# Performance work log

Measured on AMD Instinct MI355X. Metric: run time of the kernel, lower is better.

## Reference

```python
import jax, jax.numpy as jnp
import numpy as np

EMBED_DIM = 1024
NUM_HEADS = 16
HEAD_DIM = EMBED_DIM // NUM_HEADS
ROPE_THETA = 10000.0


def setup_inputs() -> dict:
    key = jax.random.key(0)
    k1, k2, k3, k4, k5 = jax.random.split(key, 5)
    B, S, E = 2, 2048, EMBED_DIM
    scale = 1.0 / np.sqrt(E)
    x = jax.random.normal(k1, (B, S, E), dtype=jnp.float32)
    w_qkv = jax.random.normal(k2, (E, 3 * E), dtype=jnp.float32) * scale
    b_qkv = jnp.zeros((3 * E,), dtype=jnp.float32)
    w_o = jax.random.normal(k3, (E, E), dtype=jnp.float32) * scale
    b_o = jnp.zeros((E,), dtype=jnp.float32)
    return {"x": x, "w_qkv": w_qkv, "b_qkv": b_qkv, "w_o": w_o, "b_o": b_o}


def _rope_cos_sin(seq_len, dtype):
    # half-dim frequencies, GPT-NeoX rotate-half convention
    inv_freq = 1.0 / (ROPE_THETA ** (jnp.arange(0, HEAD_DIM, 2, dtype=jnp.float32) / HEAD_DIM))
    pos = jnp.arange(seq_len, dtype=jnp.float32)
    freqs = pos[:, None] * inv_freq[None, :]          # [S, hd/2]
    emb = jnp.concatenate([freqs, freqs], axis=-1)    # [S, hd]
    return jnp.cos(emb).astype(dtype), jnp.sin(emb).astype(dtype)


def _rotate_half(t):
    t1, t2 = jnp.split(t, 2, axis=-1)
    return jnp.concatenate([-t2, t1], axis=-1)


def reference(x, w_qkv, b_qkv, w_o, b_o):
    B, S, E = x.shape
    H, D = NUM_HEADS, HEAD_DIM
    qkv = x @ w_qkv + b_qkv                            # [B, S, 3E]
    q, k, v = jnp.split(qkv, 3, axis=-1)
    # [B, H, S, D]
    q = q.reshape(B, S, H, D).transpose(0, 2, 1, 3)
    k = k.reshape(B, S, H, D).transpose(0, 2, 1, 3)
    v = v.reshape(B, S, H, D).transpose(0, 2, 1, 3)
    cos, sin = _rope_cos_sin(S, x.dtype)               # [S, D]
    q = q * cos + _rotate_half(q) * sin
    k = k * cos + _rotate_half(k) * sin
    scores = jnp.einsum('bhqd,bhkd->bhqk', q, k) / jnp.sqrt(jnp.asarray(D, x.dtype))
    causal = jnp.tril(jnp.ones((S, S), dtype=bool))
    scores = jnp.where(causal, scores, jnp.asarray(-1e30, x.dtype))
    attn = jax.nn.softmax(scores, axis=-1)
    out = jnp.einsum('bhqk,bhkd->bhqd', attn, v)       # [B, H, S, D]
    out = out.transpose(0, 2, 1, 3).reshape(B, S, E)
    return out @ w_o + b_o
```

## Files before the change

### kernel.cpp

```cpp
#include <hip/hip_runtime.h>
#include <hip/hip_bf16.h>

typedef __hip_bfloat16 bf16_t;
typedef __attribute__((ext_vector_type(8))) __bf16 bf16x8;
typedef __attribute__((ext_vector_type(4))) float f32x4;
typedef __attribute__((ext_vector_type(4))) unsigned short ushort4v;
typedef __attribute__((ext_vector_type(4))) short short4v;

#define NUM_B 2
#define NUM_H 16
#define SEQ   2048
#define EMB   1024
#define LOG2E 1.44269504088896340736f
#define LN10K 13.287712379549449f

__global__ __launch_bounds__(256) void prep_kernel(
    const float* __restrict__ x, const float* __restrict__ wq,
    const float* __restrict__ wo, bf16_t* __restrict__ xb,
    bf16_t* __restrict__ wqT, bf16_t* __restrict__ woT) {
  __shared__ float tile[32][33];
  int bid = blockIdx.x, tid = threadIdx.x;
  if (bid < 4096) {
    int i = (bid * 256 + tid) * 4;
    f32x4 v = *(const f32x4*)&x[i];
    ushort4v p;
#pragma unroll
    for (int j = 0; j < 4; ++j)
      p[j] = __builtin_bit_cast(unsigned short, __float2bfloat16(v[j]));
    *(ushort4v*)&xb[i] = p;
    return;
  }
  const float* src;
  bf16_t* dst;
  int R, C, c0, r0;
  if (bid < 4096 + 3072) {
    int b = bid - 4096;
    src = wq; dst = wqT; R = 1024; C = 3072;
    c0 = (b % 96) * 32; r0 = (b / 96) * 32;
  } else {
    int b = bid - 7168;
    src = wo; dst = woT; R = 1024; C = 1024;
    c0 = (b % 32) * 32; r0 = (b / 32) * 32;
  }
  int tx = tid & 31, ty = tid >> 5;
#pragma unroll
  for (int i = 0; i < 4; ++i)
    tile[ty + i * 8][tx] = src[(size_t)(r0 + ty + i * 8) * C + c0 + tx];
  __syncthreads();
#pragma unroll
  for (int i = 0; i < 4; ++i)
    dst[(size_t)(c0 + ty + i * 8) * R + r0 + tx] = __float2bfloat16(tile[tx][ty + i * 8]);
}

__device__ __forceinline__ void stage_half(const bf16_t* __restrict__ G,
                                           int row0, int k0, int ld,
                                           bf16_t* Ls, int tid) {
#pragma unroll
  for (int r = 0; r < 2; ++r) {
    int c = tid + r * 512;
    int row = c >> 3, g = c & 7;
    const char* gp = (const char*)(G + (size_t)(row0 + row) * ld + k0) +
                     ((g ^ (row & 7)) * 16);
    char* lp = (char*)Ls + c * 16;
    __builtin_amdgcn_global_load_lds((const __attribute__((address_space(1))) void*)gp,
                                     (__attribute__((address_space(3))) void*)lp, 16, 0, 0);
  }
}

__global__ __launch_bounds__(512, 2) void gemm_qkv_8ph(
    const bf16_t* __restrict__ A, const bf16_t* __restrict__ Bt,
    const float* __restrict__ bias, bf16_t* __restrict__ out0,
    bf16_t* __restrict__ out1, bf16_t* __restrict__ out2) {
  __shared__ __align__(16) bf16_t As[2][256 * 64];
  __shared__ __align__(16) bf16_t Bs[2][256 * 64];
  const int Kd = 1024;
  const int NT = 16;
  int tid = threadIdx.x;
  int wave = tid >> 6, lane = tid & 63;
  int lr = lane & 15, lq = lane >> 4;
  int wm = wave >> 2, wn = wave & 3;
  int m0 = blockIdx.x * 256, n0 = blockIdx.y * 256;
  int sw = lr & 7;
  int gk0 = (lq ^ sw) * 16;
  int gk1 = ((4 + lq) ^ sw) * 16;

  f32x4 acc[8][4];
#pragma unroll
  for (int i = 0; i < 8; ++i)
#pragma unroll
    for (int j = 0; j < 4; ++j) acc[i][j] = (f32x4){0.f, 0.f, 0.f, 0.f};

  stage_half(A, m0, 0, Kd, &As[0][0], tid);
  stage_half(A, m0 + 128, 0, Kd, &As[0][128 * 64], tid);
  stage_half(Bt, n0, 0, Kd, &Bs[0][0], tid);
  stage_half(Bt, n0 + 128, 0, Kd, &Bs[0][128 * 64], tid);
  stage_half(A, m0, 64, Kd, &As[1][0], tid);
  asm volatile("s_waitcnt vmcnt(2)" ::: "memory");
  __builtin_amdgcn_s_barrier();

  bf16x8 af[4][2], blo[2][2], bhi[2][2];
  int aw = wm * 128, bw = wn * 64;

#pragma unroll 2
  for (int t = 0; t < NT; ++t) {
    int cur = t & 1, nxt = cur ^ 1;
    const char* Ac = (const char*)As[cur];
    const char* Bc = (const char*)Bs[cur];

#pragma unroll
    for (int mi = 0; mi < 4; ++mi) {
      int ro = (aw + mi * 16 + lr) * 128;
      af[mi][0] = *(const bf16x8*)(Ac + ro + gk0);
      af[mi][1] = *(const bf16x8*)(Ac + ro + gk1);
    }
#pragma unroll
    for (int nj = 0; nj < 2; ++nj) {
      int ro = (bw + nj * 16 + lr) * 128;
      blo[nj][0] = *(const bf16x8*)(Bc + ro + gk0);
      blo[nj][1] = *(const bf16x8*)(Bc + ro + gk1);
    }
    if (t + 1 < NT) stage_half(A, m0 + 128, (t + 1) * 64, Kd, &As[nxt][128 * 64], tid);
    __builtin_amdgcn_s_barrier();
    asm volatile("s_waitcnt lgkmcnt(0)" ::: "memory");
    __builtin_amdgcn_s_setprio(1);
#pragma unroll
    for (int mi = 0; mi < 4; ++mi)
#pragma unroll
      for (int nj = 0; nj < 2; ++nj) {
        acc[mi][nj] = __builtin_amdgcn_mfma_f32_16x16x32_bf16(af[mi][0], blo[nj][0], acc[mi][nj], 0, 0, 0);
        acc[mi][nj] = __builtin_amdgcn_mfma_f32_16x16x32_bf16(af[mi][1], blo[nj][1], acc[mi][nj], 0, 0, 0);
      }
    __builtin_amdgcn_s_setprio(0);
    __builtin_amdgcn_s_barrier();

#pragma unroll
    for (int nj = 0; nj < 2; ++nj) {
      int ro = (bw + (nj + 2) * 16 + lr) * 128;
      bhi[nj][0] = *(const bf16x8*)(Bc + ro + gk0);
      bhi[nj][1] = *(const bf16x8*)(Bc + ro + gk1);
    }
    if (t + 1 < NT) stage_half(Bt, n0, (t + 1) * 64, Kd, &Bs[nxt][0], tid);
    __builtin_amdgcn_s_barrier();
    asm volatile("s_waitcnt lgkmcnt(0)" ::: "memory");
    __builtin_amdgcn_s_setprio(1);
#pragma unroll
    for (int mi = 0; mi < 4; ++mi)
#pragma unroll
      for (int nj = 0; nj < 2; ++nj) {
        acc[mi][nj + 2] = __builtin_amdgcn_mfma_f32_16x16x32_bf16(af[mi][0], bhi[nj][0], acc[mi][nj + 2], 0, 0, 0);
        acc[mi][nj + 2] = __builtin_amdgcn_mfma_f32_16x16x32_bf16(af[mi][1], bhi[nj][1], acc[mi][nj + 2], 0, 0, 0);
      }
    __builtin_amdgcn_s_setprio(0);
    __builtin_amdgcn_s_barrier();

#pragma unroll
    for (int mi = 0; mi < 4; ++mi) {
      int ro = (aw + (mi + 4) * 16 + lr) * 128;
      af[mi][0] = *(const bf16x8*)(Ac + ro + gk0);
      af[mi][1] = *(const bf16x8*)(Ac + ro + gk1);
    }
    if (t + 1 < NT) stage_half(Bt, n0 + 128, (t + 1) * 64, Kd, &Bs[nxt][128 * 64], tid);
    __builtin_amdgcn_s_barrier();
    asm volatile("s_waitcnt lgkmcnt(0)" ::: "memory");
    __builtin_amdgcn_s_setprio(1);
#pragma unroll
    for (int mi = 0; mi < 4; ++mi)
#pragma unroll
      for (int nj = 0; nj < 2; ++nj) {
        acc[mi + 4][nj + 2] = __builtin_amdgcn_mfma_f32_16x16x32_bf16(af[mi][0], bhi[nj][0], acc[mi + 4][nj + 2], 0, 0, 0);
        acc[mi + 4][nj + 2] = __builtin_amdgcn_mfma_f32_16x16x32_bf16(af[mi][1], bhi[nj][1], acc[mi + 4][nj + 2], 0, 0, 0);
      }
    __builtin_amdgcn_s_setprio(0);
    __builtin_amdgcn_s_barrier();

#pragma unroll
    for (int nj = 0; nj < 2; ++nj) {
      int ro = (bw + nj * 16 + lr) * 128;
      blo[nj][0] = *(const bf16x8*)(Bc + ro + gk0);
      blo[nj][1] = *(const bf16x8*)(Bc + ro + gk1);
    }
    if (t + 2 < NT) stage_half(A, m0, (t + 2) * 64, Kd, &As[cur][0], tid);
    __builtin_amdgcn_s_barrier();
    asm volatile("s_waitcnt lgkmcnt(0)" ::: "memory");
    __builtin_amdgcn_s_setprio(1);
#pragma unroll
    for (int mi = 0; mi < 4; ++mi)
#pragma unroll
      for (int nj = 0; nj < 2; ++nj) {
        acc[mi + 4][nj] = __builtin_amdgcn_mfma_f32_16x16x32_bf16(af[mi][0], blo[nj][0], acc[mi + 4][nj], 0, 0, 0);
        acc[mi + 4][nj] = __builtin_amdgcn_mfma_f32_16x16x32_bf16(af[mi][1], blo[nj][1], acc[mi + 4][nj], 0, 0, 0);
      }
    __builtin_amdgcn_s_setprio(0);
    if (t + 1 < NT) {
      if (t + 2 < NT) asm volatile("s_waitcnt vmcnt(2)" ::: "memory");
      else            asm volatile("s_waitcnt vmcnt(0)" ::: "memory");
      __builtin_amdgcn_s_barrier();
    }
  }

#pragma unroll
  for (int pr = 0; pr < 2; ++pr) {
    int na = n0 + wn * 64 + pr * 16 + lr;
    int nb = na + 32;
    int sec = na >> 10;
    int h = (na >> 6) & (NUM_H - 1);
    int da = na & 63;
    float bva = bias[na], bvb = bias[nb];
    if (sec == 2) {
#pragma unroll
      for (int mi = 0; mi < 8; ++mi) {
        int mbase = m0 + wm * 128 + mi * 16 + lq * 4;
        int b = mbase >> 11;
        int s = mbase & (SEQ - 1);
        int bh = b * NUM_H + h;
        ushort4v pa, pb;
#pragma unroll
        for (int r = 0; r < 4; ++r) {
          pa[r] = __builtin_bit_cast(unsigned short, __float2bfloat16(acc[mi][pr][r] + bva));
          pb[r] = __builtin_bit_cast(unsigned short, __float2bfloat16(acc[mi][pr + 2][r] + bvb));
        }
        *(ushort4v*)&out2[((size_t)bh * 64 + da) * SEQ + s] = pa;
        *(ushort4v*)&out2[((size_t)bh * 64 + da + 32) * SEQ + s] = pb;
      }
    } else {
      bf16_t* dst = (sec == 0) ? out0 : out1;
      float scale = (sec == 0) ? 0.125f : 1.0f;
      int i = da & 31;
      float inv = exp2f(-(float)i * (LN10K / 32.0f));
#pragma unroll
      for (int mi = 0; mi < 8; ++mi) {
        int mbase = m0 + wm * 128 + mi * 16 + lq * 4;
        int b = mbase >> 11;
        int s0 = mbase & (SEQ - 1);
        int bh = b * NUM_H + h;
#pragma unroll
        for (int r = 0; r < 4; ++r) {
          float sn, cs;
          sincosf((float)(s0 + r) * inv, &sn, &cs);
          float va = acc[mi][pr][r] + bva;
          float vb = acc[mi][pr + 2][r] + bvb;
          float oa = (va * cs - vb * sn) * scale;
          float ob = (vb * cs + va * sn) * scale;
          size_t rowb = ((size_t)bh * SEQ + (s0 + r)) * 64;
          dst[rowb + da] = __float2bfloat16(oa);
          dst[rowb + da + 32] = __float2bfloat16(ob);
        }
      }
    }
  }
}

template <int CH>
__device__ __forceinline__ void stage_tile(const bf16_t* __restrict__ G,
                                           int row0, int col0, int ld,
                                           bf16_t* Ls, int tid) {
#pragma unroll
  for (int r = 0; r < CH; ++r) {
    int c = tid + r * 256;
    int row = c >> 2, g = c & 3;
    const char* gp = (const char*)(G + (size_t)(row0 + row) * ld + col0) +
                     ((g ^ ((row >> 1) & 3)) * 16);
    char* lp = (char*)Ls + c * 16;
    __builtin_amdgcn_global_load_lds((const __attribute__((address_space(1))) void*)gp,
                                     (__attribute__((address_space(3))) void*)lp, 16, 0, 0);
  }
}

template <int MODE, int MT>
__global__ __launch_bounds__(256) void gemm_bf16_kernel(
    const bf16_t* __restrict__ A, const bf16_t* __restrict__ Bt,
    const float* __restrict__ bias, bf16_t* __restrict__ out0,
    bf16_t* __restrict__ out1, bf16_t* __restrict__ out2,
    float* __restrict__ outf, int Ndim, int Kdim) {
  __shared__ __align__(16) bf16_t As[MT * 32 * 32];
  __shared__ __align__(16) bf16_t Bs[128 * 32];
  int tid = threadIdx.x;
  int wave = tid >> 6, lane = tid & 63;
  int lr = lane & 15, lq = lane >> 4;
  int m0 = blockIdx.x * (32 * MT), n0 = blockIdx.y * 128;
  int wm = (wave >> 1) * (MT * 16), wn = (wave & 1) * 64;
  int key = (lr >> 1) & 3;
  int goff = ((lq ^ key) * 8);
  f32x4 acc[MT][4];
#pragma unroll
  for (int i = 0; i < MT; ++i)
#pragma unroll
    for (int j = 0; j < 4; ++j) acc[i][j] = (f32x4){0.f, 0.f, 0.f, 0.f};

  for (int k0 = 0; k0 < Kdim; k0 += 32) {
    __syncthreads();
    stage_tile<MT / 2>(A, m0, k0, Kdim, As, tid);
    stage_tile<2>(Bt, n0, k0, Kdim, Bs, tid);
    __syncthreads();
    bf16x8 af[MT], bfr[4];
#pragma unroll
    for (int mt = 0; mt < MT; ++mt)
      af[mt] = *(const bf16x8*)&As[(wm + mt * 16 + lr) * 32 + goff];
#pragma unroll
    for (int nt = 0; nt < 4; ++nt)
      bfr[nt] = *(const bf16x8*)&Bs[(wn + nt * 16 + lr) * 32 + goff];
#pragma unroll
    for (int mt = 0; mt < MT; ++mt)
#pragma unroll
      for (int nt = 0; nt < 4; ++nt)
        acc[mt][nt] = __builtin_amdgcn_mfma_f32_16x16x32_bf16(af[mt], bfr[nt], acc[mt][nt], 0, 0, 0);
  }

  if (MODE == 0) {
#pragma unroll
    for (int pr = 0; pr < 2; ++pr) {
      int na = n0 + wn + pr * 16 + lr;
      int nb = na + 32;
      int sec = na >> 10;
      int h = (na >> 6) & (NUM_H - 1);
      int da = na & 63;
      float bva = bias[na], bvb = bias[nb];
      if (sec == 2) {
#pragma unroll
        for (int mt = 0; mt < MT; ++mt) {
          int mbase = m0 + wm + mt * 16 + lq * 4;
          int b = mbase >> 11;
          int s = mbase & (SEQ - 1);
          int bh = b * NUM_H + h;
          ushort4v pa, pb;
#pragma unroll
          for (int r = 0; r < 4; ++r) {
            pa[r] = __builtin_bit_cast(unsigned short, __float2bfloat16(acc[mt][pr][r] + bva));
            pb[r] = __builtin_bit_cast(unsigned short, __float2bfloat16(acc[mt][pr + 2][r] + bvb));
          }
          *(ushort4v*)&out2[((size_t)bh * 64 + da) * SEQ + s] = pa;
          *(ushort4v*)&out2[((size_t)bh * 64 + da + 32) * SEQ + s] = pb;
        }
      } else {
        bf16_t* dst = (sec == 0) ? out0 : out1;
        float scale = (sec == 0) ? 0.125f : 1.0f;
        int i = da & 31;
        float inv = exp2f(-(float)i * (LN10K / 32.0f));
#pragma unroll
        for (int mt = 0; mt < MT; ++mt) {
          int mbase = m0 + wm + mt * 16 + lq * 4;
          int b = mbase >> 11;
          int s0 = mbase & (SEQ - 1);
          int bh = b * NUM_H + h;
#pragma unroll
          for (int r = 0; r < 4; ++r) {
            float sn, cs;
            sincosf((float)(s0 + r) * inv, &sn, &cs);
            float va = acc[mt][pr][r] + bva;
            float vb = acc[mt][pr + 2][r] + bvb;
            float oa = (va * cs - vb * sn) * scale;
            float ob = (vb * cs + va * sn) * scale;
            size_t rowb = ((size_t)bh * SEQ + (s0 + r)) * 64;
            dst[rowb + da] = __float2bfloat16(oa);
            dst[rowb + da + 32] = __float2bfloat16(ob);
          }
        }
      }
    }
  } else {
#pragma unroll
    for (int nt = 0; nt < 4; ++nt) {
      int n = n0 + wn + nt * 16 + lr;
      float bv = bias[n];
#pragma unroll
      for (int mt = 0; mt < MT; ++mt)
#pragma unroll
        for (int r = 0; r < 4; ++r) {
          int m = m0 + wm + mt * 16 + lq * 4 + r;
          outf[(size_t)m * Ndim + n] = acc[mt][nt][r] + bv;
        }
    }
  }
}

__device__ __forceinline__ void stage_sw(const char* __restrict__ gbase,
                                         size_t rowStride, bf16_t* lds, int tid) {
#pragma unroll
  for (int r = 0; r < 2; ++r) {
    int c = tid + r * 256;
    int row = c >> 3, g = c & 7;
    const char* gp = gbase + (size_t)row * rowStride + ((g ^ (row & 7)) * 16);
    char* lp = (char*)lds + c * 16;
    __builtin_amdgcn_global_load_lds((const __attribute__((address_space(1))) void*)gp,
                                     (__attribute__((address_space(3))) void*)lp, 16, 0, 0);
  }
}

__global__ __launch_bounds__(256) void flash_attn_kernel(
    const bf16_t* __restrict__ Q, const bf16_t* __restrict__ K,
    const bf16_t* __restrict__ Vt, bf16_t* __restrict__ O) {
  __shared__ __align__(16) bf16_t Ks[2][64 * 64];
  __shared__ __align__(16) bf16_t Vs[2][64 * 64];
  int tid = threadIdx.x;
  int wv = tid >> 6, lane = tid & 63;
  int lr = lane & 15, lq = lane >> 4;
  int bx = blockIdx.x;
  int bh = bx & 31;
  int tile = 31 - (bx >> 5);
  int qw0 = tile * 64 + wv * 16;
  const bf16_t* Qb = Q + (size_t)bh * SEQ * 64;
  const bf16_t* Kb = K + (size_t)bh * SEQ * 64;
  const bf16_t* Vb = Vt + (size_t)bh * 64 * SEQ;
  int sw = lr & 7;
  int g0 = (lq ^ sw) * 8;
  int g1 = g0 ^ 32;

  bf16x8 aq0 = *(const bf16x8*)&Qb[(size_t)(qw0 + lr) * 64 + lq * 8];
  bf16x8 aq1 = *(const bf16x8*)&Qb[(size_t)(qw0 + lr) * 64 + 32 + lq * 8];

  f32x4 Oacc[4];
#pragma unroll
  for (int dt = 0; dt < 4; ++dt) Oacc[dt] = (f32x4){0.f, 0.f, 0.f, 0.f};
  float lrow = 0.f;

  int nch = tile + 1;
  stage_sw((const char*)Kb, 128, Ks[0], tid);
  stage_sw((const char*)Vb, SEQ * 2, Vs[0], tid);

  for (int ch = 0; ch < nch; ++ch) {
    int cur = ch & 1;
    bool diag = (ch == tile);
    __syncthreads();
    if (ch + 1 < nch) {
      int kvn = (ch + 1) * 64;
      stage_sw((const char*)(Kb + (size_t)kvn * 64), 128, Ks[cur ^ 1], tid);
      stage_sw((const char*)Vb + (size_t)kvn * 2, SEQ * 2, Vs[cur ^ 1], tid);
    }

#pragma unroll
    for (int sub = 0; sub < 4; ++sub) {
      if (!diag || sub <= wv) {
        int rk = (sub * 16 + lr) * 64;
        bf16x8 k0 = *(const bf16x8*)&Ks[cur][rk + g0];
        bf16x8 k1 = *(const bf16x8*)&Ks[cur][rk + g1];
        f32x4 t = (f32x4){0.f, 0.f, 0.f, 0.f};
        t = __builtin_amdgcn_mfma_f32_16x16x32_bf16(k0, aq0, t, 0, 0, 0);
        t = __builtin_amdgcn_mfma_f32_16x16x32_bf16(k1, aq1, t, 0, 0, 0);
        if (diag && sub == wv) {
#pragma unroll
          for (int r = 0; r < 4; ++r)
            if (lq * 4 + r > lr) t[r] = -1e30f;
        }
        short4v pp;
#pragma unroll
        for (int r = 0; r < 4; ++r) {
          float p = exp2f(t[r] * LOG2E);
          lrow += p;
          pp[r] = __builtin_bit_cast(short, __float2bfloat16(p));
        }
#pragma unroll
        for (int dt = 0; dt < 4; ++dt) {
          int row = dt * 16 + lr;
          int grp = (sub * 2 + (lq >> 1)) ^ sw;
          short4v av = *(const short4v*)&Vs[cur][row * 64 + grp * 8 + (lq & 1) * 4];
          Oacc[dt] = __builtin_amdgcn_mfma_f32_16x16x16bf16_1k(av, pp, Oacc[dt], 0, 0, 0);
        }
      }
    }
  }

  lrow += __shfl_xor(lrow, 16, 64);
  lrow += __shfl_xor(lrow, 32, 64);

  int b = bh >> 4, h = bh & (NUM_H - 1);
  int q = qw0 + lr;
  size_t base = (((size_t)b * SEQ + q) * NUM_H + h) * 64;
  float rinv = 1.0f / lrow;
#pragma unroll
  for (int dt = 0; dt < 4; ++dt) {
    ushort4v ok;
#pragma unroll
    for (int r = 0; r < 4; ++r)
      ok[r] = __builtin_bit_cast(unsigned short, __float2bfloat16(Oacc[dt][r] * rinv));
    *(ushort4v*)&O[base + dt * 16 + lq * 4] = ok;
  }
}

extern "C" void kernel_launch(void* const* d_in, const int* in_sizes, int n_in,
                              void* d_out, int out_size, void* d_ws, size_t ws_size,
                              hipStream_t stream) {
  const float* x      = (const float*)d_in[0];
  const float* w_qkv  = (const float*)d_in[1];
  const float* b_qkv  = (const float*)d_in[2];
  const float* w_o    = (const float*)d_in[3];
  const float* b_o    = (const float*)d_in[4];
  float* out = (float*)d_out;

  bf16_t* ws    = (bf16_t*)d_ws;
  bf16_t* xb    = ws;
  bf16_t* wqkvT = xb + 4 * 1024 * 1024;
  bf16_t* woT   = wqkvT + 3072 * 1024;
  bf16_t* Qb    = woT + 1024 * 1024;
  bf16_t* Kb    = Qb + 4 * 1024 * 1024;
  bf16_t* Vt    = Kb + 4 * 1024 * 1024;
  bf16_t* attn  = Vt + 4 * 1024 * 1024;

  prep_kernel<<<8192, 256, 0, stream>>>(x, w_qkv, w_o, xb, wqkvT, woT);
  gemm_qkv_8ph<<<dim3(16, 12), 512, 0, stream>>>(xb, wqkvT, b_qkv, Qb, Kb, Vt);
  flash_attn_kernel<<<1024, 256, 0, stream>>>(Qb, Kb, Vt, attn);
  gemm_bf16_kernel<1, 2><<<dim3(64, 8), 256, 0, stream>>>(
      attn, woT, b_o, nullptr, nullptr, nullptr, out, 1024, 1024);
}
```

Before: 209.7 us.

## Precompute staging addresses and rebalance QKV GEMM prefetch schedule

Replaces the generic half-tile staging helper with per-lane precomputed global and LDS pointers, so each stage is just two global_load_lds calls at fixed offsets. The prefetch schedule is rearranged: the third phase no longer issues loads, and the fourth phase issues both the next A0 and B1 halves two steps ahead. The vmcnt waits are adjusted to match, and the loop unroll is reduced to 1. The QKV epilogue is rewritten to handle both column pairs with shared index math, and the unused MODE==0 epilogue of the generic GEMM is removed. The aim is lower address arithmetic, smaller code size and better load overlap, at the risk of weaker latency hiding because more loads are outstanding at the later barrier.

```diff
diff --git a/kernel.cpp b/kernel.cpp
--- a/kernel.cpp
+++ b/kernel.cpp
@@ -52,19 +52,11 @@
     dst[(size_t)(c0 + ty + i * 8) * R + r0 + tx] = __float2bfloat16(tile[tx][ty + i * 8]);
 }
 
-__device__ __forceinline__ void stage_half(const bf16_t* __restrict__ G,
-                                           int row0, int k0, int ld,
-                                           bf16_t* Ls, int tid) {
-#pragma unroll
-  for (int r = 0; r < 2; ++r) {
-    int c = tid + r * 512;
-    int row = c >> 3, g = c & 7;
-    const char* gp = (const char*)(G + (size_t)(row0 + row) * ld + k0) +
-                     ((g ^ (row & 7)) * 16);
-    char* lp = (char*)Ls + c * 16;
-    __builtin_amdgcn_global_load_lds((const __attribute__((address_space(1))) void*)gp,
-                                     (__attribute__((address_space(3))) void*)lp, 16, 0, 0);
-  }
+__device__ __forceinline__ void stage2(const char* gBase, int kByte, char* ldsLane) {
+  __builtin_amdgcn_global_load_lds((const __attribute__((address_space(1))) void*)(gBase + kByte),
+                                   (__attribute__((address_space(3))) void*)ldsLane, 16, 0, 0);
+  __builtin_amdgcn_global_load_lds((const __attribute__((address_space(1))) void*)(gBase + kByte + 64 * 2048),
+                                   (__attribute__((address_space(3))) void*)(ldsLane + 8192), 16, 0, 0);
 }
 
 __global__ __launch_bounds__(512, 2) void gemm_qkv_8ph(
@@ -73,7 +65,6 @@
     bf16_t* __restrict__ out1, bf16_t* __restrict__ out2) {
   __shared__ __align__(16) bf16_t As[2][256 * 64];
   __shared__ __align__(16) bf16_t Bs[2][256 * 64];
-  const int Kd = 1024;
   const int NT = 16;
   int tid = threadIdx.x;
   int wave = tid >> 6, lane = tid & 63;
@@ -84,28 +75,40 @@
   int gk0 = (lq ^ sw) * 16;
   int gk1 = ((4 + lq) ^ sw) * 16;
 
+  int rowL = tid >> 3, g7 = tid & 7;
+  size_t laneOff = (size_t)rowL * 2048 + ((g7 ^ (rowL & 7)) * 16);
+  const char* A0L = (const char*)(A + (size_t)m0 * 1024) + laneOff;
+  const char* A1L = A0L + 128 * 2048;
+  const char* B0L = (const char*)(Bt + (size_t)n0 * 1024) + laneOff;
+  const char* B1L = B0L + 128 * 2048;
+  char* AsL = (char*)As + (size_t)tid * 16;
+  char* BsL = (char*)Bs + (size_t)tid * 16;
+
   f32x4 acc[8][4];
 #pragma unroll
   for (int i = 0; i < 8; ++i)
 #pragma unroll
     for (int j = 0; j < 4; ++j) acc[i][j] = (f32x4){0.f, 0.f, 0.f, 0.f};
 
-  stage_half(A, m0, 0, Kd, &As[0][0], tid);
-  stage_half(A, m0 + 128, 0, Kd, &As[0][128 * 64], tid);
-  stage_half(Bt, n0, 0, Kd, &Bs[0][0], tid);
-  stage_half(Bt, n0 + 128, 0, Kd, &Bs[0][128 * 64], tid);
-  stage_half(A, m0, 64, Kd, &As[1][0], tid);
-  asm volatile("s_waitcnt vmcnt(2)" ::: "memory");
+  stage2(A0L, 0, AsL);
+  stage2(A1L, 0, AsL + 16384);
+  stage2(B0L, 0, BsL);
+  stage2(B1L, 0, BsL + 16384);
+  stage2(A0L, 128, AsL + 32768);
+  stage2(B1L, 128, BsL + 32768 + 16384);
+  asm volatile("s_waitcnt vmcnt(4)" ::: "memory");
   __builtin_amdgcn_s_barrier();
 
   bf16x8 af[4][2], blo[2][2], bhi[2][2];
   int aw = wm * 128, bw = wn * 64;
 
-#pragma unroll 2
+#pragma unroll 1
   for (int t = 0; t < NT; ++t) {
     int cur = t & 1, nxt = cur ^ 1;
-    const char* Ac = (const char*)As[cur];
-    const char* Bc = (const char*)Bs[cur];
+    const char* Ac = (const char*)As + cur * 32768;
+    const char* Bc = (const char*)Bs + cur * 32768;
+    int kbN = (t + 1) * 128;
+    int kbN2 = (t + 2) * 128;
 
 #pragma unroll
     for (int mi = 0; mi < 4; ++mi) {
@@ -119,7 +122,7 @@
       blo[nj][0] = *(const bf16x8*)(Bc + ro + gk0);
       blo[nj][1] = *(const bf16x8*)(Bc + ro + gk1);
     }
-    if (t + 1 < NT) stage_half(A, m0 + 128, (t + 1) * 64, Kd, &As[nxt][128 * 64], tid);
+    if (t + 1 < NT) stage2(A1L, kbN, AsL + nxt * 32768 + 16384);
     __builtin_amdgcn_s_barrier();
     asm volatile("s_waitcnt lgkmcnt(0)" ::: "memory");
     __builtin_amdgcn_s_setprio(1);
@@ -139,7 +142,7 @@
       bhi[nj][0] = *(const bf16x8*)(Bc + ro + gk0);
       bhi[nj][1] = *(const bf16x8*)(Bc + ro + gk1);
     }
-    if (t + 1 < NT) stage_half(Bt, n0, (t + 1) * 64, Kd, &Bs[nxt][0], tid);
+    if (t + 1 < NT) stage2(B0L, kbN, BsL + nxt * 32768);
     __builtin_amdgcn_s_barrier();
     asm volatile("s_waitcnt lgkmcnt(0)" ::: "memory");
     __builtin_amdgcn_s_setprio(1);
@@ -159,7 +162,6 @@
       af[mi][0] = *(const bf16x8*)(Ac + ro + gk0);
       af[mi][1] = *(const bf16x8*)(Ac + ro + gk1);
     }
-    if (t + 1 < NT) stage_half(Bt, n0 + 128, (t + 1) * 64, Kd, &Bs[nxt][128 * 64], tid);
     __builtin_amdgcn_s_barrier();
     asm volatile("s_waitcnt lgkmcnt(0)" ::: "memory");
     __builtin_amdgcn_s_setprio(1);
@@ -179,7 +181,10 @@
       blo[nj][0] = *(const bf16x8*)(Bc + ro + gk0);
       blo[nj][1] = *(const bf16x8*)(Bc + ro + gk1);
     }
-    if (t + 2 < NT) stage_half(A, m0, (t + 2) * 64, Kd, &As[cur][0], tid);
+    if (t + 2 < NT) {
+      stage2(A0L, kbN2, AsL + cur * 32768);
+      stage2(B1L, kbN2, BsL + cur * 32768 + 16384);
+    }
     __builtin_amdgcn_s_barrier();
     asm volatile("s_waitcnt lgkmcnt(0)" ::: "memory");
     __builtin_amdgcn_s_setprio(1);
@@ -192,59 +197,60 @@
       }
     __builtin_amdgcn_s_setprio(0);
     if (t + 1 < NT) {
-      if (t + 2 < NT) asm volatile("s_waitcnt vmcnt(2)" ::: "memory");
+      if (t + 2 < NT) asm volatile("s_waitcnt vmcnt(4)" ::: "memory");
       else            asm volatile("s_waitcnt vmcnt(0)" ::: "memory");
       __builtin_amdgcn_s_barrier();
     }
   }
 
-#pragma unroll
-  for (int pr = 0; pr < 2; ++pr) {
-    int na = n0 + wn * 64 + pr * 16 + lr;
-    int nb = na + 32;
-    int sec = na >> 10;
-    int h = (na >> 6) & (NUM_H - 1);
-    int da = na & 63;
-    float bva = bias[na], bvb = bias[nb];
-    if (sec == 2) {
-#pragma unroll
-      for (int mi = 0; mi < 8; ++mi) {
-        int mbase = m0 + wm * 128 + mi * 16 + lq * 4;
-        int b = mbase >> 11;
-        int s = mbase & (SEQ - 1);
-        int bh = b * NUM_H + h;
-        ushort4v pa, pb;
-#pragma unroll
-        for (int r = 0; r < 4; ++r) {
-          pa[r] = __builtin_bit_cast(unsigned short, __float2bfloat16(acc[mi][pr][r] + bva));
-          pb[r] = __builtin_bit_cast(unsigned short, __float2bfloat16(acc[mi][pr + 2][r] + bvb));
-        }
-        *(ushort4v*)&out2[((size_t)bh * 64 + da) * SEQ + s] = pa;
-        *(ushort4v*)&out2[((size_t)bh * 64 + da + 32) * SEQ + s] = pb;
-      }
-    } else {
-      bf16_t* dst = (sec == 0) ? out0 : out1;
-      float scale = (sec == 0) ? 0.125f : 1.0f;
-      int i = da & 31;
-      float inv = exp2f(-(float)i * (LN10K / 32.0f));
-#pragma unroll
-      for (int mi = 0; mi < 8; ++mi) {
-        int mbase = m0 + wm * 128 + mi * 16 + lq * 4;
-        int b = mbase >> 11;
-        int s0 = mbase & (SEQ - 1);
-        int bh = b * NUM_H + h;
-#pragma unroll
-        for (int r = 0; r < 4; ++r) {
-          float sn, cs;
-          sincosf((float)(s0 + r) * inv, &sn, &cs);
-          float va = acc[mi][pr][r] + bva;
-          float vb = acc[mi][pr + 2][r] + bvb;
-          float oa = (va * cs - vb * sn) * scale;
-          float ob = (vb * cs + va * sn) * scale;
-          size_t rowb = ((size_t)bh * SEQ + (s0 + r)) * 64;
-          dst[rowb + da] = __float2bfloat16(oa);
-          dst[rowb + da + 32] = __float2bfloat16(ob);
-        }
+  int nb0 = n0 + wn * 64 + lr;
+  int sec = nb0 >> 10;
+  int h = (nb0 >> 6) & (NUM_H - 1);
+  float bva0 = bias[nb0],      bvb0 = bias[nb0 + 32];
+  float bva1 = bias[nb0 + 16], bvb1 = bias[nb0 + 48];
+  if (sec == 2) {
+#pragma unroll
+    for (int mi = 0; mi < 8; ++mi) {
+      int mbase = m0 + wm * 128 + mi * 16 + lq * 4;
+      int b = mbase >> 11;
+      int s = mbase & (SEQ - 1);
+      size_t bh64 = ((size_t)(b * NUM_H + h)) * 64;
+      ushort4v pa0, pb0, pa1, pb1;
+#pragma unroll
+      for (int r = 0; r < 4; ++r) {
+        pa0[r] = __builtin_bit_cast(unsigned short, __float2bfloat16(acc[mi][0][r] + bva0));
+        pb0[r] = __builtin_bit_cast(unsigned short, __float2bfloat16(acc[mi][2][r] + bvb0));
+        pa1[r] = __builtin_bit_cast(unsigned short, __float2bfloat16(acc[mi][1][r] + bva1));
+        pb1[r] = __builtin_bit_cast(unsigned short, __float2bfloat16(acc[mi][3][r] + bvb1));
+      }
+      *(ushort4v*)&out2[(bh64 + lr) * SEQ + s] = pa0;
+      *(ushort4v*)&out2[(bh64 + lr + 32) * SEQ + s] = pb0;
+      *(ushort4v*)&out2[(bh64 + lr + 16) * SEQ + s] = pa1;
+      *(ushort4v*)&out2[(bh64 + lr + 48) * SEQ + s] = pb1;
+    }
+  } else {
+    bf16_t* dst = (sec == 0) ? out0 : out1;
+    float scale = (sec == 0) ? 0.125f : 1.0f;
+    float inv0 = exp2f(-(float)lr * (LN10K / 32.0f));
+    float inv1 = exp2f(-(float)(lr + 16) * (LN10K / 32.0f));
+#pragma unroll
+    for (int mi = 0; mi < 8; ++mi) {
+      int mbase = m0 + wm * 128 + mi * 16 + lq * 4;
+      int b = mbase >> 11;
+      int s0 = mbase & (SEQ - 1);
+      int bh = b * NUM_H + h;
+#pragma unroll
+      for (int r = 0; r < 4; ++r) {
+        float sn0, cs0, sn1, cs1;
+        sincosf((float)(s0 + r) * inv0, &sn0, &cs0);
+        sincosf((float)(s0 + r) * inv1, &sn1, &cs1);
+        float va0 = acc[mi][0][r] + bva0, vb0 = acc[mi][2][r] + bvb0;
+        float va1 = acc[mi][1][r] + bva1, vb1 = acc[mi][3][r] + bvb1;
+        size_t rowb = ((size_t)bh * SEQ + (s0 + r)) * 64;
+        dst[rowb + lr]      = __float2bfloat16((va0 * cs0 - vb0 * sn0) * scale);
+        dst[rowb + lr + 32] = __float2bfloat16((vb0 * cs0 + va0 * sn0) * scale);
+        dst[rowb + lr + 16] = __float2bfloat16((va1 * cs1 - vb1 * sn1) * scale);
+        dst[rowb + lr + 48] = __float2bfloat16((vb1 * cs1 + va1 * sn1) * scale);
       }
     }
   }
@@ -306,58 +312,7 @@
         acc[mt][nt] = __builtin_amdgcn_mfma_f32_16x16x32_bf16(af[mt], bfr[nt], acc[mt][nt], 0, 0, 0);
   }
 
-  if (MODE == 0) {
-#pragma unroll
-    for (int pr = 0; pr < 2; ++pr) {
-      int na = n0 + wn + pr * 16 + lr;
-      int nb = na + 32;
-      int sec = na >> 10;
-      int h = (na >> 6) & (NUM_H - 1);
-      int da = na & 63;
-      float bva = bias[na], bvb = bias[nb];
-      if (sec == 2) {
-#pragma unroll
-        for (int mt = 0; mt < MT; ++mt) {
-          int mbase = m0 + wm + mt * 16 + lq * 4;
-          int b = mbase >> 11;
-          int s = mbase & (SEQ - 1);
-          int bh = b * NUM_H + h;
-          ushort4v pa, pb;
-#pragma unroll
-          for (int r = 0; r < 4; ++r) {
-            pa[r] = __builtin_bit_cast(unsigned short, __float2bfloat16(acc[mt][pr][r] + bva));
-            pb[r] = __builtin_bit_cast(unsigned short, __float2bfloat16(acc[mt][pr + 2][r] + bvb));
-          }
-          *(ushort4v*)&out2[((size_t)bh * 64 + da) * SEQ + s] = pa;
-          *(ushort4v*)&out2[((size_t)bh * 64 + da + 32) * SEQ + s] = pb;
-        }
-      } else {
-        bf16_t* dst = (sec == 0) ? out0 : out1;
-        float scale = (sec == 0) ? 0.125f : 1.0f;
-        int i = da & 31;
-        float inv = exp2f(-(float)i * (LN10K / 32.0f));
-#pragma unroll
-        for (int mt = 0; mt < MT; ++mt) {
-          int mbase = m0 + wm + mt * 16 + lq * 4;
-          int b = mbase >> 11;
-          int s0 = mbase & (SEQ - 1);
-          int bh = b * NUM_H + h;
-#pragma unroll
-          for (int r = 0; r < 4; ++r) {
-            float sn, cs;
-            sincosf((float)(s0 + r) * inv, &sn, &cs);
-            float va = acc[mt][pr][r] + bva;
-            float vb = acc[mt][pr + 2][r] + bvb;
-            float oa = (va * cs - vb * sn) * scale;
-            float ob = (vb * cs + va * sn) * scale;
-            size_t rowb = ((size_t)bh * SEQ + (s0 + r)) * 64;
-            dst[rowb + da] = __float2bfloat16(oa);
-            dst[rowb + da + 32] = __float2bfloat16(ob);
-          }
-        }
-      }
-    }
-  } else {
+  if (MODE == 1) {
 #pragma unroll
     for (int nt = 0; nt < 4; ++nt) {
       int n = n0 + wn + nt * 16 + lr;
```

Measured after the change: 205.4 us. 1.02x faster.
